# Optimization experiments

Hardware: AMD Instinct MI355X
Metric: run time of the kernel (lower is better)

## Reference

```python
import jax, jax.numpy as jnp
import numpy as np

NUM_GRAPHS = 256


def gcn_conv(x, W, b, src, dst, n_nodes):
    """PyG GCNConv: add self-loops, symmetric normalization, linear transform."""
    h = x @ W  # [N, out]
    loop = jnp.arange(n_nodes, dtype=src.dtype)
    src_f = jnp.concatenate([src, loop])  # messages j -> i, with self-loops
    dst_f = jnp.concatenate([dst, loop])
    deg = jax.ops.segment_sum(jnp.ones_like(src_f, dtype=h.dtype), dst_f,
                              num_segments=n_nodes)  # in-degree incl. self-loop
    dinv = jnp.where(deg > 0, jax.lax.rsqrt(deg), 0.0)
    norm = dinv[src_f] * dinv[dst_f]  # [E+N]
    msg = h[src_f] * norm[:, None]  # gather + scale, [E+N, out]
    out = jax.ops.segment_sum(msg, dst_f, num_segments=n_nodes)  # scatter-add
    return out + b


def global_mean_pool(x, batch, num_graphs):
    sums = jax.ops.segment_sum(x, batch, num_segments=num_graphs)
    cnt = jax.ops.segment_sum(jnp.ones((x.shape[0],), x.dtype), batch,
                              num_segments=num_graphs)
    return sums / jnp.maximum(cnt, 1.0)[:, None]


def setup_inputs() -> dict:
    key = jax.random.key(0)
    k = jax.random.split(key, 6)
    N, E, D = 50000, 800000, 133
    x = jax.random.normal(k[0], (N, D), dtype=jnp.float32)
    edge_index = jax.random.randint(k[1], (2, E), 0, N, dtype=jnp.int64)
    batch = jnp.sort(jax.random.randint(k[2], (N,), 0, NUM_GRAPHS, dtype=jnp.int64))
    s = 1.0 / np.sqrt(D)
    W1 = jax.random.normal(k[3], (D, D), dtype=jnp.float32) * s
    b1 = jnp.zeros((D,), jnp.float32)
    W2 = jax.random.normal(k[4], (D, D), dtype=jnp.float32) * s
    b2 = jnp.zeros((D,), jnp.float32)
    return {"x": x, "edge_index": edge_index, "batch": batch,
            "W1": W1, "b1": b1, "W2": W2, "b2": b2}


def reference(x, edge_index, batch, W1, b1, W2, b2):
    n = x.shape[0]
    src, dst = edge_index[0], edge_index[1]
    h = jax.nn.relu(gcn_conv(x, W1, b1, src, dst, n))
    h = jax.nn.relu(gcn_conv(h, W2, b2, src, dst, n))
    return global_mean_pool(h, batch, NUM_GRAPHS)  # [num_graphs, 133]
```

## Files before the change

### kernel.cpp

```cpp
#include <hip/hip_runtime.h>

#define D 133
#define DPB 160
#define NCGB 17
#define NGRAPH 256
#define KS 168
#define LSTR 168
#define NT 9
#define CAP 64

typedef short short8 __attribute__((ext_vector_type(8)));
typedef float float4v __attribute__((ext_vector_type(4)));

__device__ __forceinline__ unsigned short f2bf(float x) {
    unsigned int u = __float_as_uint(x);
    u += 0x7fffu + ((u >> 16) & 1u);
    return (unsigned short)(u >> 16);
}

__device__ __forceinline__ void cvt8(uint4 v, float* f) {
    f[0] = __uint_as_float(v.x << 16);
    f[1] = __uint_as_float(v.x & 0xffff0000u);
    f[2] = __uint_as_float(v.y << 16);
    f[3] = __uint_as_float(v.y & 0xffff0000u);
    f[4] = __uint_as_float(v.z << 16);
    f[5] = __uint_as_float(v.z & 0xffff0000u);
    f[6] = __uint_as_float(v.w << 16);
    f[7] = __uint_as_float(v.w & 0xffff0000u);
}

__global__ __launch_bounds__(256) void k_wt(const float* __restrict__ W1,
                                            unsigned short* __restrict__ WT1,
                                            const float* __restrict__ W2,
                                            unsigned short* __restrict__ WT2,
                                            int* __restrict__ cnt,
                                            const int* __restrict__ batch,
                                            int* __restrict__ gstart,
                                            int N, int wtB, int czB) {
    int bid = blockIdx.x, t = threadIdx.x;
    if (bid < 2 * wtB) {
        const float* W = (bid < wtB) ? W1 : W2;
        unsigned short* WT = (bid < wtB) ? WT1 : WT2;
        int lb = (bid < wtB) ? bid : bid - wtB;
        int i = lb * 256 + t;
        if (i < 144 * KS) {
            int n = i / KS, k = i - n * KS;
            WT[i] = (n < D && k < D) ? f2bf(W[(size_t)k * D + n]) : (unsigned short)0;
        }
        return;
    }
    bid -= 2 * wtB;
    if (bid < czB) {
        int i = bid * 256 + t;
        if (i < N) cnt[i] = 0;
        return;
    }
    bid -= czB;
    {
        int g = bid * 256 + t;
        if (g > NGRAPH) return;
        int lo = 0, hi = N;
        while (lo < hi) {
            int mid = (lo + hi) >> 1;
            if (batch[mid] < g) lo = mid + 1; else hi = mid;
        }
        gstart[g] = lo;
    }
}

__global__ __launch_bounds__(256, 2) void k_big(const float* __restrict__ X,
                                                const unsigned short* __restrict__ WTg,
                                                unsigned short* __restrict__ Y,
                                                const int* __restrict__ src,
                                                const int* __restrict__ dst,
                                                int* __restrict__ cnt,
                                                unsigned short* __restrict__ earr,
                                                int N, int E, int mt) {
    int bid = blockIdx.x, t = threadIdx.x;
    int g = bid / 5, pos = bid - g * 5;
    if (pos != 4) {
        int i = (g * 4 + pos) * 256 + t;
        if (i < E) {
            int s = src[i];
            int dnode = dst[i];
            int slot = atomicAdd(&cnt[dnode], 1);
            if (slot < CAP) earr[(size_t)dnode * CAP + slot] = (unsigned short)s;
        }
        return;
    }
    int wave = t >> 6, lane = t & 63;
    int ln16 = lane & 15, quad = lane >> 4;
    int tile = g * 4 + wave;
    if (tile >= mt) return;
    int row0 = tile * 16;
    int ra = row0 + ln16; if (ra > N - 1) ra = N - 1;
    const float* Xr = X + (size_t)ra * D;
    const unsigned short* Wr = WTg + (size_t)ln16 * KS + quad * 8;

    float4v acc[NT];
    #pragma unroll
    for (int n = 0; n < NT; ++n) acc[n] = {0.f, 0.f, 0.f, 0.f};

    #pragma unroll
    for (int kk = 0; kk < 5; ++kk) {
        int cbase = kk * 32 + quad * 8;
        short8 a;
        if (kk < 4) {
            #pragma unroll
            for (int j = 0; j < 8; ++j) a[j] = (short)f2bf(Xr[cbase + j]);
        } else {
            #pragma unroll
            for (int j = 0; j < 8; ++j) {
                int c = cbase + j;
                a[j] = (short)((c < D) ? f2bf(Xr[c]) : 0);
            }
        }
        #pragma unroll
        for (int n = 0; n < NT; ++n) {
            short8 b = *(const short8*)(Wr + n * 16 * KS + kk * 32);
            acc[n] = __builtin_amdgcn_mfma_f32_16x16x32_bf16(a, b, acc[n], 0, 0, 0);
        }
    }
    #pragma unroll
    for (int r = 0; r < 4; ++r) {
        int row = row0 + quad * 4 + r;
        if (row < N) {
            unsigned short* Yr = Y + (size_t)row * DPB + ln16;
            #pragma unroll
            for (int n = 0; n < NT; ++n) Yr[n * 16] = f2bf(acc[n][r]);
        }
    }
}

__global__ __launch_bounds__(320, 2) void k_aggmm(const unsigned short* __restrict__ H,
                                                  const float* __restrict__ bias,
                                                  const int* __restrict__ cnt,
                                                  const unsigned short* __restrict__ earr,
                                                  const unsigned short* __restrict__ WTg,
                                                  unsigned short* __restrict__ Y, int N) {
    __shared__ unsigned short T[16 * LSTR];
    int t = threadIdx.x;
    int row0 = blockIdx.x * 16;
    if (t < 272) {
        int l = t / NCGB;
        int cg = t - l * NCGB;
        int node = row0 + l;
        if (node >= N) node = N - 1;
        int c = cg << 3;
        int degraw = cnt[node];
        float di = rsqrtf((float)(degraw + 1));
        float acc[8], f[8];
        uint4 hv = *(const uint4*)(H + (size_t)node * DPB + c);
        cvt8(hv, f);
        #pragma unroll
        for (int j = 0; j < 8; ++j) acc[j] = di * f[j];
        int deg = degraw > CAP ? CAP : degraw;
        const unsigned short* ep = earr + (size_t)node * CAP;
        int e = 0;
        for (; e + 4 <= deg; e += 4) {
            int s0 = ep[e], s1 = ep[e+1], s2 = ep[e+2], s3 = ep[e+3];
            float w0 = rsqrtf((float)(cnt[s0] + 1));
            float w1 = rsqrtf((float)(cnt[s1] + 1));
            float w2 = rsqrtf((float)(cnt[s2] + 1));
            float w3 = rsqrtf((float)(cnt[s3] + 1));
            uint4 v0 = *(const uint4*)(H + (size_t)s0 * DPB + c);
            uint4 v1 = *(const uint4*)(H + (size_t)s1 * DPB + c);
            uint4 v2 = *(const uint4*)(H + (size_t)s2 * DPB + c);
            uint4 v3 = *(const uint4*)(H + (size_t)s3 * DPB + c);
            cvt8(v0, f);
            #pragma unroll
            for (int j = 0; j < 8; ++j) acc[j] = fmaf(w0, f[j], acc[j]);
            cvt8(v1, f);
            #pragma unroll
            for (int j = 0; j < 8; ++j) acc[j] = fmaf(w1, f[j], acc[j]);
            cvt8(v2, f);
            #pragma unroll
            for (int j = 0; j < 8; ++j) acc[j] = fmaf(w2, f[j], acc[j]);
            cvt8(v3, f);
            #pragma unroll
            for (int j = 0; j < 8; ++j) acc[j] = fmaf(w3, f[j], acc[j]);
        }
        for (; e < deg; ++e) {
            int s = ep[e];
            float wv = rsqrtf((float)(cnt[s] + 1));
            uint4 v = *(const uint4*)(H + (size_t)s * DPB + c);
            cvt8(v, f);
            #pragma unroll
            for (int j = 0; j < 8; ++j) acc[j] = fmaf(wv, f[j], acc[j]);
        }
        float b[8];
        #pragma unroll
        for (int j = 0; j < 8; ++j) b[j] = (c + j < D) ? bias[c + j] : 0.f;
        unsigned int p[4];
        #pragma unroll
        for (int j = 0; j < 4; ++j) {
            float lo = fmaxf(fmaf(di, acc[2*j],   b[2*j]),   0.f);
            float hi = fmaxf(fmaf(di, acc[2*j+1], b[2*j+1]), 0.f);
            p[j] = (unsigned int)f2bf(lo) | ((unsigned int)f2bf(hi) << 16);
        }
        uint4 pk = {p[0], p[1], p[2], p[3]};
        *(uint4*)(T + l * LSTR + c) = pk;
    } else {
        int k = t - 272;
        int l = k / 3, seg = k - l * 3;
        uint4 z = {0u, 0u, 0u, 0u};
        *(uint4*)(T + l * LSTR + 136 + seg * 8) = z;
    }
    __syncthreads();

    int wave = t >> 6, lane = t & 63;
    int ln16 = lane & 15, quad = lane >> 4;
    const unsigned short* Ar = T + ln16 * LSTR + quad * 8;
    const unsigned short* Wr = WTg + (size_t)ln16 * KS + quad * 8;
    for (int n = wave; n < NT; n += 5) {
        float4v acc2 = {0.f, 0.f, 0.f, 0.f};
        #pragma unroll
        for (int kk = 0; kk < 5; ++kk) {
            short8 a = *(const short8*)(Ar + kk * 32);
            short8 b = *(const short8*)(Wr + n * 16 * KS + kk * 32);
            acc2 = __builtin_amdgcn_mfma_f32_16x16x32_bf16(a, b, acc2, 0, 0, 0);
        }
        #pragma unroll
        for (int r = 0; r < 4; ++r) {
            int row = row0 + quad * 4 + r;
            if (row < N) Y[(size_t)row * DPB + n * 16 + ln16] = f2bf(acc2[r]);
        }
    }
}

__global__ __launch_bounds__(256) void k_agg2(const unsigned short* __restrict__ H,
                                              const float* __restrict__ bias,
                                              const int* __restrict__ cnt,
                                              const unsigned short* __restrict__ earr,
                                              unsigned short* __restrict__ outb, int N) {
    int idx = blockIdx.x * 256 + threadIdx.x;
    if (idx >= N * NCGB) return;
    int node = idx / NCGB;
    int cg = idx - node * NCGB;
    int c = cg << 3;
    int degraw = cnt[node];
    float di = rsqrtf((float)(degraw + 1));
    float acc[8], f[8];
    uint4 hv = *(const uint4*)(H + (size_t)node * DPB + c);
    cvt8(hv, f);
    #pragma unroll
    for (int j = 0; j < 8; ++j) acc[j] = di * f[j];
    int deg = degraw > CAP ? CAP : degraw;
    const unsigned short* ep = earr + (size_t)node * CAP;
    int e = 0;
    for (; e + 4 <= deg; e += 4) {
        int s0 = ep[e], s1 = ep[e+1], s2 = ep[e+2], s3 = ep[e+3];
        float w0 = rsqrtf((float)(cnt[s0] + 1));
        float w1 = rsqrtf((float)(cnt[s1] + 1));
        float w2 = rsqrtf((float)(cnt[s2] + 1));
        float w3 = rsqrtf((float)(cnt[s3] + 1));
        uint4 v0 = *(const uint4*)(H + (size_t)s0 * DPB + c);
        uint4 v1 = *(const uint4*)(H + (size_t)s1 * DPB + c);
        uint4 v2 = *(const uint4*)(H + (size_t)s2 * DPB + c);
        uint4 v3 = *(const uint4*)(H + (size_t)s3 * DPB + c);
        cvt8(v0, f);
        #pragma unroll
        for (int j = 0; j < 8; ++j) acc[j] = fmaf(w0, f[j], acc[j]);
        cvt8(v1, f);
        #pragma unroll
        for (int j = 0; j < 8; ++j) acc[j] = fmaf(w1, f[j], acc[j]);
        cvt8(v2, f);
        #pragma unroll
        for (int j = 0; j < 8; ++j) acc[j] = fmaf(w2, f[j], acc[j]);
        cvt8(v3, f);
        #pragma unroll
        for (int j = 0; j < 8; ++j) acc[j] = fmaf(w3, f[j], acc[j]);
    }
    for (; e < deg; ++e) {
        int s = ep[e];
        float wv = rsqrtf((float)(cnt[s] + 1));
        uint4 v = *(const uint4*)(H + (size_t)s * DPB + c);
        cvt8(v, f);
        #pragma unroll
        for (int j = 0; j < 8; ++j) acc[j] = fmaf(wv, f[j], acc[j]);
    }
    float b[8];
    #pragma unroll
    for (int j = 0; j < 8; ++j) b[j] = (c + j < D) ? bias[c + j] : 0.f;
    unsigned int p[4];
    #pragma unroll
    for (int j = 0; j < 4; ++j) {
        float lo = fmaxf(fmaf(di, acc[2*j],   b[2*j]),   0.f);
        float hi = fmaxf(fmaf(di, acc[2*j+1], b[2*j+1]), 0.f);
        p[j] = (unsigned int)f2bf(lo) | ((unsigned int)f2bf(hi) << 16);
    }
    uint4 pk = {p[0], p[1], p[2], p[3]};
    *(uint4*)(outb + (size_t)node * DPB + c) = pk;
}

__global__ __launch_bounds__(256) void k_pool(const unsigned short* __restrict__ H,
                                              const int* __restrict__ gstart,
                                              float* __restrict__ out) {
    int g = blockIdx.x / NCGB;
    int cg = blockIdx.x - g * NCGB;
    int c = cg << 3;
    int t = threadIdx.x;
    int s = gstart[g], e = gstart[g + 1];
    float acc[8], f[8];
    #pragma unroll
    for (int j = 0; j < 8; ++j) acc[j] = 0.f;
    for (int i = s + t; i < e; i += 256) {
        uint4 v = *(const uint4*)(H + (size_t)i * DPB + c);
        cvt8(v, f);
        #pragma unroll
        for (int j = 0; j < 8; ++j) acc[j] += f[j];
    }
    #pragma unroll
    for (int off = 32; off >= 1; off >>= 1) {
        #pragma unroll
        for (int j = 0; j < 8; ++j) acc[j] += __shfl_down(acc[j], off, 64);
    }
    __shared__ float part[4][8];
    int wave = t >> 6, lane = t & 63;
    if (lane == 0) {
        #pragma unroll
        for (int j = 0; j < 8; ++j) part[wave][j] = acc[j];
    }
    __syncthreads();
    if (t < 8) {
        int col = c + t;
        if (col < D) {
            float v = part[0][t] + part[1][t] + part[2][t] + part[3][t];
            float n = (float)(e - s);
            out[(size_t)g * D + col] = v / fmaxf(n, 1.f);
        }
    }
}

extern "C" void kernel_launch(void* const* d_in, const int* in_sizes, int n_in,
                              void* d_out, int out_size, void* d_ws, size_t ws_size,
                              hipStream_t stream) {
    const float* x   = (const float*)d_in[0];
    const int* ei    = (const int*)d_in[1];
    const int* batch = (const int*)d_in[2];
    const float* W1  = (const float*)d_in[3];
    const float* b1  = (const float*)d_in[4];
    const float* W2  = (const float*)d_in[5];
    const float* b2  = (const float*)d_in[6];
    float* out = (float*)d_out;

    int N = in_sizes[0] / D;
    int E = in_sizes[1] / 2;
    const int* src = ei;
    const int* dst = ei + E;

    char* w = (char*)d_ws;
    unsigned short* HbA = (unsigned short*)w; w += (size_t)N * DPB * 2;
    unsigned short* HbB = (unsigned short*)w; w += (size_t)N * DPB * 2;
    int* cnt            = (int*)w;            w += (size_t)N * 4;
    unsigned short* earr= (unsigned short*)w; w += (size_t)N * CAP * 2;
    int* gstart         = (int*)w;            w += (size_t)(NGRAPH + 1) * 4;
    unsigned short* WT1 = (unsigned short*)w; w += (size_t)144 * KS * 2;
    unsigned short* WT2 = (unsigned short*)w; w += (size_t)144 * KS * 2;

    int wtB = (144 * KS + 255) / 256;
    int czB = (N + 255) / 256;
    int gsB = (NGRAPH + 1 + 255) / 256;

    int mt = (N + 15) / 16;
    int mmB = (mt + 3) / 4;
    int nib = 5 * mmB;
    int grid_agg = (N * NCGB + 255) / 256;

    k_wt    <<<2 * wtB + czB + gsB, 256, 0, stream>>>(W1, WT1, W2, WT2, cnt,
                                                      batch, gstart, N, wtB, czB);
    k_big   <<<nib, 256, 0, stream>>>(x, WT1, HbA, src, dst, cnt, earr, N, E, mt);
    k_aggmm <<<mt, 320, 0, stream>>>(HbA, b1, cnt, earr, WT2, HbB, N);
    k_agg2  <<<grid_agg, 256, 0, stream>>>(HbB, b2, cnt, earr, HbA, N);
    k_pool  <<<NGRAPH * NCGB, 256, 0, stream>>>(HbA, gstart, out);
}
```

Measured before the change: 249.5 us.

## Partition edge-bucketing by destination range across blocks with vectorized dst loads

The edge-fill work in the fused kernel is now split into 8 destination-node ranges. Each group of blocks scans every edge but only atomically inserts edges whose destination falls in its range. The aim is to localize atomics and earr writes, with the hardware scheduling co-resident blocks, so L2 traffic is less scattered. Each thread handles 8 edges using int4 loads of dst. The cost is reading the dst array 8 times, and the matmul blocks are no longer interleaved with fill blocks but placed after all of them.

```diff
diff --git a/kernel.cpp b/kernel.cpp
--- a/kernel.cpp
+++ b/kernel.cpp
@@ -8,6 +8,7 @@
 #define LSTR 168
 #define NT 9
 #define CAP 64
+#define EU 8
 
 typedef short short8 __attribute__((ext_vector_type(8)));
 typedef float float4v __attribute__((ext_vector_type(4)));
@@ -75,22 +76,40 @@
                                                 const int* __restrict__ dst,
                                                 int* __restrict__ cnt,
                                                 unsigned short* __restrict__ earr,
-                                                int N, int E, int mt) {
+                                                int N, int E, int mt, int nfill) {
     int bid = blockIdx.x, t = threadIdx.x;
-    int g = bid / 5, pos = bid - g * 5;
-    if (pos != 4) {
-        int i = (g * 4 + pos) * 256 + t;
-        if (i < E) {
-            int s = src[i];
-            int dnode = dst[i];
-            int slot = atomicAdd(&cnt[dnode], 1);
-            if (slot < CAP) earr[(size_t)dnode * CAP + slot] = (unsigned short)s;
+    if (bid < nfill) {
+        int g = bid & 7;
+        int chunk = bid >> 3;
+        int rlo = g * (N >> 3);
+        int rhi = (g == 7) ? N : rlo + (N >> 3);
+        int i0 = (chunk * 256 + t) * EU;
+        if (i0 >= E) return;
+        int dv[EU];
+        if (i0 + EU <= E) {
+            int4 a = *(const int4*)(dst + i0);
+            int4 b = *(const int4*)(dst + i0 + 4);
+            dv[0]=a.x; dv[1]=a.y; dv[2]=a.z; dv[3]=a.w;
+            dv[4]=b.x; dv[5]=b.y; dv[6]=b.z; dv[7]=b.w;
+        } else {
+            #pragma unroll
+            for (int j = 0; j < EU; ++j) dv[j] = (i0 + j < E) ? dst[i0 + j] : -1;
+        }
+        #pragma unroll
+        for (int j = 0; j < EU; ++j) {
+            int dnode = dv[j];
+            if (dnode >= rlo && dnode < rhi) {
+                int s = src[i0 + j];
+                int slot = atomicAdd(&cnt[dnode], 1);
+                if (slot < CAP) earr[(size_t)dnode * CAP + slot] = (unsigned short)s;
+            }
         }
         return;
     }
+    bid -= nfill;
     int wave = t >> 6, lane = t & 63;
     int ln16 = lane & 15, quad = lane >> 4;
-    int tile = g * 4 + wave;
+    int tile = bid * 4 + wave;
     if (tile >= mt) return;
     int row0 = tile * 16;
     int ra = row0 + ln16; if (ra > N - 1) ra = N - 1;
@@ -364,12 +383,14 @@
 
     int mt = (N + 15) / 16;
     int mmB = (mt + 3) / 4;
-    int nib = 5 * mmB;
+    int chunks = (E + 256 * EU - 1) / (256 * EU);
+    int nfill = 8 * chunks;
     int grid_agg = (N * NCGB + 255) / 256;
 
     k_wt    <<<2 * wtB + czB + gsB, 256, 0, stream>>>(W1, WT1, W2, WT2, cnt,
                                                       batch, gstart, N, wtB, czB);
-    k_big   <<<nib, 256, 0, stream>>>(x, WT1, HbA, src, dst, cnt, earr, N, E, mt);
+    k_big   <<<nfill + mmB, 256, 0, stream>>>(x, WT1, HbA, src, dst, cnt, earr,
+                                              N, E, mt, nfill);
     k_aggmm <<<mt, 320, 0, stream>>>(HbA, b1, cnt, earr, WT2, HbB, N);
     k_agg2  <<<grid_agg, 256, 0, stream>>>(HbB, b2, cnt, earr, HbA, N);
     k_pool  <<<NGRAPH * NCGB, 256, 0, stream>>>(HbA, gstart, out);
```

New measurement: 258.9 us. 1.04x slower.
